# Kernel tuning notes

Measured on AMD Instinct MI355X. Metric: run time of the kernel, lower is better.

The kernel has to match this reference:

```python
import jax, jax.numpy as jnp
import numpy as np

B = 64        # number of jagged segments
LMAX = 1024   # max_seq_len
D = 512       # input feature dim
K = 512       # output feature dim
NW = 128      # number of selectable weight matrices
T = 32768     # total jagged tokens (avg len 512)


def setup_inputs() -> dict:
    rng = np.random.default_rng(0)
    # Monotone offsets with avg segment length T//B = 512, jittered +/-200
    # so every length stays in (0, LMAX].
    offsets = np.arange(B + 1, dtype=np.int64) * (T // B)
    offsets[1:-1] += rng.integers(-200, 200, size=B - 1)
    key = jax.random.key(0)
    k1, k2, k3, k4 = jax.random.split(key, 4)
    jagged = jax.random.normal(k1, (T, D), dtype=jnp.float32)
    weight = jax.random.normal(k2, (NW, D, K), dtype=jnp.float32) * 0.02
    bias = jax.random.normal(k3, (NW, K), dtype=jnp.float32)
    index = jax.random.randint(k4, (B,), 0, NW)
    return {
        "max_seq_len": LMAX,
        "offsets": jnp.asarray(offsets),
        "index": index,
        "jagged": jagged,
        "weight": weight,
        "bias": bias,
    }


def reference(max_seq_len, offsets, index, jagged, weight, bias):
    # out[offsets[b]:offsets[b+1]] = jagged[offsets[b]:offsets[b+1]] @ weight[index[b]] + bias[index[b]]
    T_, Dd = jagged.shape
    Kk = weight.shape[-1]
    starts = offsets[:-1]            # [B]
    ends = offsets[1:]               # [B]
    pos = starts[:, None] + jnp.arange(max_seq_len)[None, :]   # [B, L] global row ids
    valid = pos < ends[:, None]                                # [B, L]
    safe = jnp.where(valid, pos, 0)
    padded = jnp.where(valid[..., None], jagged[safe], 0)      # [B, L, D]
    w = weight[index]                                          # [B, D, K] (index-select)
    b = bias[index]                                            # [B, K]
    out_p = jnp.einsum("bld,bdk->blk", padded, w) + b[:, None, :]  # [B, L, K]
    # Scatter padded result back to jagged layout; invalid slots go to row T_ (dropped).
    scatter_idx = jnp.where(valid, pos, T_)
    out = jnp.zeros((T_ + 1, Kk), jagged.dtype).at[scatter_idx].set(out_p)
    return out[:T_]
```

## Files before the change

kernel.cpp:

```cpp
#include <hip/hip_runtime.h>
#include <hip/hip_bf16.h>

#define D_DIM 512
#define K_DIM 512
#define B_C   64
#define LMAX_C 1024

#define BM 128
#define BN 128
#define BK 64
#define KSTEPS 8
#define ROWT 8
#define COLT 4
#define NWG  (B_C * ROWT * COLT)

typedef __attribute__((ext_vector_type(8))) short bf16x8;
typedef __attribute__((ext_vector_type(4))) float f32x4;

__device__ __forceinline__ short f2bf(float f) {
    union { __hip_bfloat16 h; short s; } u;
    u.h = __float2bfloat16(f);
    return u.s;
}

__device__ __forceinline__ short* lds_addr(short* base, int row, int kbyte) {
    return (short*)((char*)base + row * 128 +
                    (kbyte ^ ((((row & 7) ^ ((row >> 2) & 7))) << 4)));
}

__global__ __launch_bounds__(256, 2) void jbmm_kernel(
    const int* __restrict__ offsets,
    const int* __restrict__ index,
    const float* __restrict__ jagged,
    const float* __restrict__ weight,
    const float* __restrict__ bias,
    float* __restrict__ out)
{
    __shared__ short As[2][BM * BK];
    __shared__ short Bs[2][BN * BK];

    const int bidRaw = blockIdx.x;
    const int bid = (bidRaw & 7) * (NWG / 8) + (bidRaw >> 3);

    const int b   = bid / (ROWT * COLT);
    const int rt  = (bid / COLT) % ROWT;
    const int ct  = bid % COLT;

    const int start = offsets[b];
    const int end   = offsets[b + 1];
    const int m0    = start + rt * BM;
    if (m0 >= end) return;
    const int rows = (end - m0) < BM ? (end - m0) : BM;

    const int idxw = index[b];
    const float* W = weight + (size_t)idxw * D_DIM * K_DIM;
    const int n0 = ct * BN;

    const int tid  = threadIdx.x;
    const int lane = tid & 63;
    const int wid  = tid >> 6;
    const int wr   = wid >> 1;
    const int wc   = wid & 1;
    const int lr   = lane & 15;
    const int lg   = lane >> 4;

    const int arow  = tid >> 3;
    const int acol8 = tid & 7;
    const int n4    = tid & 31;
    const int dq8   = tid >> 5;

    float bias_v[4];
#pragma unroll
    for (int ni = 0; ni < 4; ++ni)
        bias_v[ni] = bias[(size_t)idxw * K_DIM + n0 + wc * 64 + ni * 16 + lr];

    f32x4 acc[4][4];
#pragma unroll
    for (int mi = 0; mi < 4; ++mi)
#pragma unroll
        for (int ni = 0; ni < 4; ++ni)
            acc[mi][ni] = (f32x4){0.f, 0.f, 0.f, 0.f};

    f32x4 aR[8];
    f32x4 bR[8];

#define LOADA(k0_)                                                          \
    {                                                                       \
        _Pragma("unroll")                                                   \
        for (int i = 0; i < 4; ++i) {                                       \
            const int r = arow + 32 * i;                                    \
            f32x4 v0 = (f32x4){0.f,0.f,0.f,0.f};                            \
            f32x4 v1 = (f32x4){0.f,0.f,0.f,0.f};                            \
            if (r < rows) {                                                 \
                const float* p = &jagged[(size_t)(m0 + r) * D_DIM + (k0_) + acol8 * 8]; \
                v0 = *reinterpret_cast<const f32x4*>(p);                    \
                v1 = *reinterpret_cast<const f32x4*>(p + 4);                \
            }                                                               \
            aR[2 * i] = v0; aR[2 * i + 1] = v1;                             \
        }                                                                   \
    }

#define LOADB(k0_)                                                          \
    {                                                                       \
        _Pragma("unroll")                                                   \
        for (int j = 0; j < 8; ++j)                                         \
            bR[j] = *reinterpret_cast<const f32x4*>(                        \
                &W[(size_t)((k0_) + dq8 * 8 + j) * K_DIM + n0 + n4 * 4]);   \
    }

#define CVTSTORE(c_)                                                        \
    {                                                                       \
        _Pragma("unroll")                                                   \
        for (int i = 0; i < 4; ++i) {                                       \
            const int r = arow + 32 * i;                                    \
            bf16x8 w;                                                       \
            w[0] = f2bf(aR[2*i][0]); w[1] = f2bf(aR[2*i][1]);               \
            w[2] = f2bf(aR[2*i][2]); w[3] = f2bf(aR[2*i][3]);               \
            w[4] = f2bf(aR[2*i+1][0]); w[5] = f2bf(aR[2*i+1][1]);           \
            w[6] = f2bf(aR[2*i+1][2]); w[7] = f2bf(aR[2*i+1][3]);           \
            *reinterpret_cast<bf16x8*>(lds_addr(&As[c_][0], r, acol8 * 16)) = w; \
        }                                                                   \
        _Pragma("unroll")                                                   \
        for (int np = 0; np < 4; ++np) {                                    \
            bf16x8 w;                                                       \
            w[0] = f2bf(bR[0][np]); w[1] = f2bf(bR[1][np]);                 \
            w[2] = f2bf(bR[2][np]); w[3] = f2bf(bR[3][np]);                 \
            w[4] = f2bf(bR[4][np]); w[5] = f2bf(bR[5][np]);                 \
            w[6] = f2bf(bR[6][np]); w[7] = f2bf(bR[7][np]);                 \
            *reinterpret_cast<bf16x8*>(lds_addr(&Bs[c_][0], n4 * 4 + np, dq8 * 16)) = w; \
        }                                                                   \
    }

#define COMPUTE(c_)                                                         \
    {                                                                       \
        __builtin_amdgcn_s_setprio(1);                                      \
        _Pragma("unroll")                                                   \
        for (int kh = 0; kh < 2; ++kh) {                                    \
            bf16x8 af[4], bfr[4];                                           \
            _Pragma("unroll")                                               \
            for (int mi = 0; mi < 4; ++mi)                                  \
                af[mi] = *reinterpret_cast<bf16x8*>(                        \
                    lds_addr(&As[c_][0], wr * 64 + mi * 16 + lr, kh * 64 + lg * 16)); \
            _Pragma("unroll")                                               \
            for (int ni = 0; ni < 4; ++ni)                                  \
                bfr[ni] = *reinterpret_cast<bf16x8*>(                       \
                    lds_addr(&Bs[c_][0], wc * 64 + ni * 16 + lr, kh * 64 + lg * 16)); \
            _Pragma("unroll")                                               \
            for (int mi = 0; mi < 4; ++mi)                                  \
                _Pragma("unroll")                                           \
                for (int ni = 0; ni < 4; ++ni)                              \
                    acc[mi][ni] = __builtin_amdgcn_mfma_f32_16x16x32_bf16(  \
                        af[mi], bfr[ni], acc[mi][ni], 0, 0, 0);             \
        }                                                                   \
        __builtin_amdgcn_s_setprio(0);                                      \
    }

#define BARRIER_LDS()                                                       \
    {                                                                       \
        asm volatile("s_waitcnt lgkmcnt(0)" ::: "memory");                  \
        __builtin_amdgcn_s_barrier();                                       \
        asm volatile("" ::: "memory");                                      \
    }

    LOADA(0); LOADB(0);
    CVTSTORE(0);
    BARRIER_LDS();

#pragma unroll
    for (int t = 0; t < KSTEPS; ++t) {
        if (t + 1 < KSTEPS) {
            const int kn = (t + 1) * BK;
            LOADA(kn); LOADB(kn);
        }
        COMPUTE(t & 1);
        if (t + 1 < KSTEPS) {
            CVTSTORE((t + 1) & 1);
            BARRIER_LDS();
        }
    }

#pragma unroll
    for (int mi = 0; mi < 4; ++mi) {
        const int rloc = wr * 64 + mi * 16 + lg * 4;
#pragma unroll
        for (int r = 0; r < 4; ++r) {
            const int rr = rloc + r;
            if (rr < rows) {
#pragma unroll
                for (int ni = 0; ni < 4; ++ni) {
                    out[(size_t)(m0 + rr) * K_DIM + n0 + wc * 64 + ni * 16 + lr] =
                        acc[mi][ni][r] + bias_v[ni];
                }
            }
        }
    }
}

extern "C" void kernel_launch(void* const* d_in, const int* in_sizes, int n_in,
                              void* d_out, int out_size, void* d_ws, size_t ws_size,
                              hipStream_t stream) {
    const int*   offsets = (const int*)d_in[1];
    const int*   index   = (const int*)d_in[2];
    const float* jagged  = (const float*)d_in[3];
    const float* weight  = (const float*)d_in[4];
    const float* bias    = (const float*)d_in[5];
    float*       out     = (float*)d_out;

    dim3 grid(NWG);
    dim3 block(256);
    hipLaunchKernelGGL(jbmm_kernel, grid, block, 0, stream,
                       offsets, index, jagged, weight, bias, out);
}
```

Measured before the change: 46.56 us.

## Pre-convert selected weights to transposed bf16 in workspace before GEMM

```diff
diff --git a/kernel.cpp b/kernel.cpp
--- a/kernel.cpp
+++ b/kernel.cpp
@@ -4,7 +4,6 @@
 #define D_DIM 512
 #define K_DIM 512
 #define B_C   64
-#define LMAX_C 1024
 
 #define BM 128
 #define BN 128
@@ -14,6 +13,8 @@
 #define COLT 4
 #define NWG  (B_C * ROWT * COLT)
 
+#define WS_NEED ((size_t)B_C * D_DIM * K_DIM * 2)
+
 typedef __attribute__((ext_vector_type(8))) short bf16x8;
 typedef __attribute__((ext_vector_type(4))) float f32x4;
 
@@ -23,16 +24,59 @@
     return u.s;
 }
 
-__device__ __forceinline__ short* lds_addr(short* base, int row, int kbyte) {
-    return (short*)((char*)base + row * 128 +
-                    (kbyte ^ ((((row & 7) ^ ((row >> 2) & 7))) << 4)));
-}
-
-__global__ __launch_bounds__(256, 2) void jbmm_kernel(
+__device__ __forceinline__ int fS(int r) { return (r & 7) ^ ((r >> 2) & 7); }
+
+__global__ __launch_bounds__(256) void wconv_kernel(
+    const int* __restrict__ index,
+    const float* __restrict__ weight,
+    short* __restrict__ wbf)
+{
+    __shared__ float tile[64][65];
+    const int blk = blockIdx.x;
+    const int b  = blk >> 6;
+    const int nt = (blk >> 3) & 7;
+    const int kt = blk & 7;
+    const int idxw = index[b];
+    const float* W = weight + (size_t)idxw * D_DIM * K_DIM;
+
+    const int tid = threadIdx.x;
+    {
+        const int rr = tid >> 2;
+        const int rq = tid & 3;
+        f32x4 v[4];
+#pragma unroll
+        for (int j = 0; j < 4; ++j)
+            v[j] = *reinterpret_cast<const f32x4*>(
+                &W[(size_t)(kt * 64 + rr) * K_DIM + nt * 64 + rq * 16 + 4 * j]);
+#pragma unroll
+        for (int j = 0; j < 4; ++j)
+#pragma unroll
+            for (int e = 0; e < 4; ++e)
+                tile[rr][rq * 16 + 4 * j + e] = v[j][e];
+    }
+    __syncthreads();
+    {
+        const int wrow = tid >> 2;
+        const int wq   = tid & 3;
+        bf16x8 o0, o1;
+#pragma unroll
+        for (int j = 0; j < 8; ++j) o0[j] = f2bf(tile[wq * 16 + j][wrow]);
+#pragma unroll
+        for (int j = 0; j < 8; ++j) o1[j] = f2bf(tile[wq * 16 + 8 + j][wrow]);
+        short* dst = wbf + ((size_t)b << 18) +
+                     (size_t)(nt * 64 + wrow) * D_DIM + kt * 64 + wq * 16;
+        *reinterpret_cast<bf16x8*>(dst)     = o0;
+        *reinterpret_cast<bf16x8*>(dst + 8) = o1;
+    }
+}
+
+template <bool WCONV>
+__global__ __launch_bounds__(256) void jbmm_kernel(
     const int* __restrict__ offsets,
     const int* __restrict__ index,
     const float* __restrict__ jagged,
     const float* __restrict__ weight,
+    const short* __restrict__ wbf,
     const float* __restrict__ bias,
     float* __restrict__ out)
 {
@@ -54,6 +98,7 @@
 
     const int idxw = index[b];
     const float* W = weight + (size_t)idxw * D_DIM * K_DIM;
+    const short* WT = wbf + ((size_t)b << 18);
     const int n0 = ct * BN;
 
     const int tid  = threadIdx.x;
@@ -66,8 +111,10 @@
 
     const int arow  = tid >> 3;
     const int acol8 = tid & 7;
-    const int n4    = tid & 31;
-    const int dq8   = tid >> 5;
+    const int n4  = tid & 31;
+    const int dq8 = tid >> 5;
+    const int nrowB  = tid >> 1;
+    const int khalfB = tid & 1;
 
     float bias_v[4];
 #pragma unroll
@@ -82,7 +129,8 @@
             acc[mi][ni] = (f32x4){0.f, 0.f, 0.f, 0.f};
 
     f32x4 aR[8];
-    f32x4 bR[8];
+    f32x4 bRf[8];
+    bf16x8 bRh[4];
 
 #define LOADA(k0_)                                                          \
     {                                                                       \
@@ -102,10 +150,17 @@
 
 #define LOADB(k0_)                                                          \
     {                                                                       \
-        _Pragma("unroll")                                                   \
-        for (int j = 0; j < 8; ++j)                                         \
-            bR[j] = *reinterpret_cast<const f32x4*>(                        \
-                &W[(size_t)((k0_) + dq8 * 8 + j) * K_DIM + n0 + n4 * 4]);   \
+        if constexpr (WCONV) {                                              \
+            const short* p = WT + (size_t)(n0 + nrowB) * D_DIM + (k0_) + khalfB * 32; \
+            _Pragma("unroll")                                               \
+            for (int j = 0; j < 4; ++j)                                     \
+                bRh[j] = *reinterpret_cast<const bf16x8*>(p + 8 * j);       \
+        } else {                                                            \
+            _Pragma("unroll")                                               \
+            for (int j = 0; j < 8; ++j)                                     \
+                bRf[j] = *reinterpret_cast<const f32x4*>(                   \
+                    &W[(size_t)((k0_) + dq8 * 8 + j) * K_DIM + n0 + n4 * 4]); \
+        }                                                                   \
     }
 
 #define CVTSTORE(c_)                                                        \
@@ -113,21 +168,33 @@
         _Pragma("unroll")                                                   \
         for (int i = 0; i < 4; ++i) {                                       \
             const int r = arow + 32 * i;                                    \
-            bf16x8 w;                                                       \
-            w[0] = f2bf(aR[2*i][0]); w[1] = f2bf(aR[2*i][1]);               \
-            w[2] = f2bf(aR[2*i][2]); w[3] = f2bf(aR[2*i][3]);               \
-            w[4] = f2bf(aR[2*i+1][0]); w[5] = f2bf(aR[2*i+1][1]);           \
-            w[6] = f2bf(aR[2*i+1][2]); w[7] = f2bf(aR[2*i+1][3]);           \
-            *reinterpret_cast<bf16x8*>(lds_addr(&As[c_][0], r, acol8 * 16)) = w; \
-        }                                                                   \
-        _Pragma("unroll")                                                   \
-        for (int np = 0; np < 4; ++np) {                                    \
-            bf16x8 w;                                                       \
-            w[0] = f2bf(bR[0][np]); w[1] = f2bf(bR[1][np]);                 \
-            w[2] = f2bf(bR[2][np]); w[3] = f2bf(bR[3][np]);                 \
-            w[4] = f2bf(bR[4][np]); w[5] = f2bf(bR[5][np]);                 \
-            w[6] = f2bf(bR[6][np]); w[7] = f2bf(bR[7][np]);                 \
-            *reinterpret_cast<bf16x8*>(lds_addr(&Bs[c_][0], n4 * 4 + np, dq8 * 16)) = w; \
+            bf16x8 w8;                                                      \
+            w8[0] = f2bf(aR[2*i][0]); w8[1] = f2bf(aR[2*i][1]);             \
+            w8[2] = f2bf(aR[2*i][2]); w8[3] = f2bf(aR[2*i][3]);             \
+            w8[4] = f2bf(aR[2*i+1][0]); w8[5] = f2bf(aR[2*i+1][1]);         \
+            w8[6] = f2bf(aR[2*i+1][2]); w8[7] = f2bf(aR[2*i+1][3]);         \
+            *reinterpret_cast<bf16x8*>(                                     \
+                (char*)&As[c_][0] + r * 128 + ((acol8 ^ fS(r)) << 4)) = w8; \
+        }                                                                   \
+        if constexpr (WCONV) {                                              \
+            _Pragma("unroll")                                               \
+            for (int j = 0; j < 4; ++j) {                                   \
+                const int sl = (khalfB * 4 + j) ^ fS(nrowB);                \
+                *reinterpret_cast<bf16x8*>(                                 \
+                    (char*)&Bs[c_][0] + nrowB * 128 + (sl << 4)) = bRh[j];  \
+            }                                                               \
+        } else {                                                            \
+            _Pragma("unroll")                                               \
+            for (int np = 0; np < 4; ++np) {                                \
+                const int row = n4 * 4 + np;                                \
+                bf16x8 w8;                                                  \
+                w8[0] = f2bf(bRf[0][np]); w8[1] = f2bf(bRf[1][np]);         \
+                w8[2] = f2bf(bRf[2][np]); w8[3] = f2bf(bRf[3][np]);         \
+                w8[4] = f2bf(bRf[4][np]); w8[5] = f2bf(bRf[5][np]);         \
+                w8[6] = f2bf(bRf[6][np]); w8[7] = f2bf(bRf[7][np]);         \
+                *reinterpret_cast<bf16x8*>(                                 \
+                    (char*)&Bs[c_][0] + row * 128 + ((dq8 ^ fS(row)) << 4)) = w8; \
+            }                                                               \
         }                                                                   \
     }
 
@@ -138,13 +205,17 @@
         for (int kh = 0; kh < 2; ++kh) {                                    \
             bf16x8 af[4], bfr[4];                                           \
             _Pragma("unroll")                                               \
-            for (int mi = 0; mi < 4; ++mi)                                  \
+            for (int mi = 0; mi < 4; ++mi) {                                \
+                const int row = wr * 64 + mi * 16 + lr;                     \
                 af[mi] = *reinterpret_cast<bf16x8*>(                        \
-                    lds_addr(&As[c_][0], wr * 64 + mi * 16 + lr, kh * 64 + lg * 16)); \
-            _Pragma("unroll")                                               \
-            for (int ni = 0; ni < 4; ++ni)                                  \
+                    (char*)&As[c_][0] + row * 128 + (((kh * 4 + lg) ^ fS(row)) << 4)); \
+            }                                                               \
+            _Pragma("unroll")                                               \
+            for (int ni = 0; ni < 4; ++ni) {                                \
+                const int row = wc * 64 + ni * 16 + lr;                     \
                 bfr[ni] = *reinterpret_cast<bf16x8*>(                       \
-                    lds_addr(&Bs[c_][0], wc * 64 + ni * 16 + lr, kh * 64 + lg * 16)); \
+                    (char*)&Bs[c_][0] + row * 128 + (((kh * 4 + lg) ^ fS(row)) << 4)); \
+            }                                                               \
             _Pragma("unroll")                                               \
             for (int mi = 0; mi < 4; ++mi)                                  \
                 _Pragma("unroll")                                           \
@@ -205,9 +276,15 @@
     const float* weight  = (const float*)d_in[4];
     const float* bias    = (const float*)d_in[5];
     float*       out     = (float*)d_out;
-
-    dim3 grid(NWG);
-    dim3 block(256);
-    hipLaunchKernelGGL(jbmm_kernel, grid, block, 0, stream,
-                       offsets, index, jagged, weight, bias, out);
-}
+    short*       wbf     = (short*)d_ws;
+
+    if (ws_size >= WS_NEED) {
+        hipLaunchKernelGGL(wconv_kernel, dim3(B_C * 64), dim3(256), 0, stream,
+                           index, weight, wbf);
+        hipLaunchKernelGGL((jbmm_kernel<true>), dim3(NWG), dim3(256), 0, stream,
+                           offsets, index, jagged, weight, wbf, bias, out);
+    } else {
+        hipLaunchKernelGGL((jbmm_kernel<false>), dim3(NWG), dim3(256), 0, stream,
+                           offsets, index, jagged, weight, wbf, bias, out);
+    }
+}
```

Measured after the change: 59.39 us. 27.6% more time.

## Make workgroups persistent over row tiles of a segment, prefetching the next tile

Applied to the files above, without the earlier changes.

```diff
diff --git a/kernel.cpp b/kernel.cpp
--- a/kernel.cpp
+++ b/kernel.cpp
@@ -4,7 +4,6 @@
 #define D_DIM 512
 #define K_DIM 512
 #define B_C   64
-#define LMAX_C 1024
 
 #define BM 128
 #define BN 128
@@ -12,7 +11,8 @@
 #define KSTEPS 8
 #define ROWT 8
 #define COLT 4
-#define NWG  (B_C * ROWT * COLT)
+#define HALVES 2
+#define NWG  (B_C * COLT * HALVES)
 
 typedef __attribute__((ext_vector_type(8))) short bf16x8;
 typedef __attribute__((ext_vector_type(4))) float f32x4;
@@ -23,9 +23,9 @@
     return u.s;
 }
 
-__device__ __forceinline__ short* lds_addr(short* base, int row, int kbyte) {
-    return (short*)((char*)base + row * 128 +
-                    (kbyte ^ ((((row & 7) ^ ((row >> 2) & 7))) << 4)));
+__device__ __forceinline__ int fS(int r) { return (r & 7) ^ ((r >> 2) & 7); }
+__device__ __forceinline__ char* lds_addr(short* base, int row, int kbyte) {
+    return (char*)base + row * 128 + (kbyte ^ (fS(row) << 4));
 }
 
 __global__ __launch_bounds__(256, 2) void jbmm_kernel(
@@ -42,15 +42,17 @@
     const int bidRaw = blockIdx.x;
     const int bid = (bidRaw & 7) * (NWG / 8) + (bidRaw >> 3);
 
-    const int b   = bid / (ROWT * COLT);
-    const int rt  = (bid / COLT) % ROWT;
-    const int ct  = bid % COLT;
+    const int h    = bid & 1;
+    const int pair = bid >> 1;
+    const int ct   = pair & 3;
+    const int b    = pair >> 2;
 
     const int start = offsets[b];
     const int end   = offsets[b + 1];
-    const int m0    = start + rt * BM;
+    int rt = h;
+    int m0 = start + rt * BM;
     if (m0 >= end) return;
-    const int rows = (end - m0) < BM ? (end - m0) : BM;
+    int rows = (end - m0) < BM ? (end - m0) : BM;
 
     const int idxw = index[b];
     const float* W = weight + (size_t)idxw * D_DIM * K_DIM;
@@ -84,15 +86,15 @@
     f32x4 aR[8];
     f32x4 bR[8];
 
-#define LOADA(k0_)                                                          \
+#define LOADA(k0_, M0_, ROWS_)                                              \
     {                                                                       \
         _Pragma("unroll")                                                   \
         for (int i = 0; i < 4; ++i) {                                       \
             const int r = arow + 32 * i;                                    \
             f32x4 v0 = (f32x4){0.f,0.f,0.f,0.f};                            \
             f32x4 v1 = (f32x4){0.f,0.f,0.f,0.f};                            \
-            if (r < rows) {                                                 \
-                const float* p = &jagged[(size_t)(m0 + r) * D_DIM + (k0_) + acol8 * 8]; \
+            if (r < (ROWS_)) {                                              \
+                const float* p = &jagged[(size_t)((M0_) + r) * D_DIM + (k0_) + acol8 * 8]; \
                 v0 = *reinterpret_cast<const f32x4*>(p);                    \
                 v1 = *reinterpret_cast<const f32x4*>(p + 4);                \
             }                                                               \
@@ -113,21 +115,22 @@
         _Pragma("unroll")                                                   \
         for (int i = 0; i < 4; ++i) {                                       \
             const int r = arow + 32 * i;                                    \
-            bf16x8 w;                                                       \
-            w[0] = f2bf(aR[2*i][0]); w[1] = f2bf(aR[2*i][1]);               \
-            w[2] = f2bf(aR[2*i][2]); w[3] = f2bf(aR[2*i][3]);               \
-            w[4] = f2bf(aR[2*i+1][0]); w[5] = f2bf(aR[2*i+1][1]);           \
-            w[6] = f2bf(aR[2*i+1][2]); w[7] = f2bf(aR[2*i+1][3]);           \
-            *reinterpret_cast<bf16x8*>(lds_addr(&As[c_][0], r, acol8 * 16)) = w; \
+            bf16x8 w8;                                                      \
+            w8[0] = f2bf(aR[2*i][0]); w8[1] = f2bf(aR[2*i][1]);             \
+            w8[2] = f2bf(aR[2*i][2]); w8[3] = f2bf(aR[2*i][3]);             \
+            w8[4] = f2bf(aR[2*i+1][0]); w8[5] = f2bf(aR[2*i+1][1]);         \
+            w8[6] = f2bf(aR[2*i+1][2]); w8[7] = f2bf(aR[2*i+1][3]);         \
+            *reinterpret_cast<bf16x8*>(lds_addr(&As[c_][0], r, acol8 * 16)) = w8; \
         }                                                                   \
         _Pragma("unroll")                                                   \
         for (int np = 0; np < 4; ++np) {                                    \
-            bf16x8 w;                                                       \
-            w[0] = f2bf(bR[0][np]); w[1] = f2bf(bR[1][np]);                 \
-            w[2] = f2bf(bR[2][np]); w[3] = f2bf(bR[3][np]);                 \
-            w[4] = f2bf(bR[4][np]); w[5] = f2bf(bR[5][np]);                 \
-            w[6] = f2bf(bR[6][np]); w[7] = f2bf(bR[7][np]);                 \
-            *reinterpret_cast<bf16x8*>(lds_addr(&Bs[c_][0], n4 * 4 + np, dq8 * 16)) = w; \
+            const int row = n4 * 4 + np;                                    \
+            bf16x8 w8;                                                      \
+            w8[0] = f2bf(bR[0][np]); w8[1] = f2bf(bR[1][np]);               \
+            w8[2] = f2bf(bR[2][np]); w8[3] = f2bf(bR[3][np]);               \
+            w8[4] = f2bf(bR[4][np]); w8[5] = f2bf(bR[5][np]);               \
+            w8[6] = f2bf(bR[6][np]); w8[7] = f2bf(bR[7][np]);               \
+            *reinterpret_cast<bf16x8*>(lds_addr(&Bs[c_][0], row, dq8 * 16)) = w8; \
         }                                                                   \
     }
 
@@ -162,37 +165,56 @@
         asm volatile("" ::: "memory");                                      \
     }
 
-    LOADA(0); LOADB(0);
+    LOADA(0, m0, rows); LOADB(0);
     CVTSTORE(0);
     BARRIER_LDS();
 
-#pragma unroll
-    for (int t = 0; t < KSTEPS; ++t) {
-        if (t + 1 < KSTEPS) {
-            const int kn = (t + 1) * BK;
-            LOADA(kn); LOADB(kn);
+    while (true) {
+#pragma unroll
+        for (int t = 0; t < KSTEPS; ++t) {
+            if (t + 1 < KSTEPS) {
+                const int kn = (t + 1) * BK;
+                LOADA(kn, m0, rows); LOADB(kn);
+            }
+            COMPUTE(t & 1);
+            if (t + 1 < KSTEPS) {
+                CVTSTORE((t + 1) & 1);
+                BARRIER_LDS();
+            }
         }
-        COMPUTE(t & 1);
-        if (t + 1 < KSTEPS) {
-            CVTSTORE((t + 1) & 1);
-            BARRIER_LDS();
-        }
-    }
-
-#pragma unroll
-    for (int mi = 0; mi < 4; ++mi) {
-        const int rloc = wr * 64 + mi * 16 + lg * 4;
-#pragma unroll
-        for (int r = 0; r < 4; ++r) {
-            const int rr = rloc + r;
-            if (rr < rows) {
-#pragma unroll
-                for (int ni = 0; ni < 4; ++ni) {
-                    out[(size_t)(m0 + rr) * K_DIM + n0 + wc * 64 + ni * 16 + lr] =
-                        acc[mi][ni][r] + bias_v[ni];
+
+        const int rtn  = rt + HALVES;
+        const int m0n  = start + rtn * BM;
+        const bool more = (m0n < end);
+        const int rowsn = more ? ((end - m0n) < BM ? (end - m0n) : BM) : 0;
+        if (more) { LOADA(0, m0n, rowsn); LOADB(0); }
+
+#pragma unroll
+        for (int mi = 0; mi < 4; ++mi) {
+            const int rloc = wr * 64 + mi * 16 + lg * 4;
+#pragma unroll
+            for (int r = 0; r < 4; ++r) {
+                const int rr = rloc + r;
+                if (rr < rows) {
+#pragma unroll
+                    for (int ni = 0; ni < 4; ++ni) {
+                        out[(size_t)(m0 + rr) * K_DIM + n0 + wc * 64 + ni * 16 + lr] =
+                            acc[mi][ni][r] + bias_v[ni];
+                    }
                 }
             }
         }
+        if (!more) break;
+
+#pragma unroll
+        for (int mi = 0; mi < 4; ++mi)
+#pragma unroll
+            for (int ni = 0; ni < 4; ++ni)
+                acc[mi][ni] = (f32x4){0.f, 0.f, 0.f, 0.f};
+        m0 = m0n; rows = rowsn; rt = rtn;
+
+        CVTSTORE(0);
+        BARRIER_LDS();
     }
 }
 
```

Measured after the change: 120.6 us. 2.59x slower.
